# Kernel optimization log

Measured on AMD Instinct MI355X. Metric: run time of the kernel, lower is better.

## Reference

```python
import jax, jax.numpy as jnp
import numpy as np

NOPE = 128          # qk_nope_head_dim
ROPE = 64           # qk_rope_head_dim
KV_LORA = 512       # kv_lora_rank
SCALE = (KV_LORA + ROPE) ** (-0.5)


def setup_inputs() -> dict:
    key = jax.random.key(0)
    k1, k2, k3, k4, k5 = jax.random.split(key, 5)
    T, H, K, S = 512, 128, 512, 8192
    q = jax.random.normal(k1, (T, H, NOPE + ROPE), dtype=jnp.float32)
    kv_cache = jax.random.normal(k2, (S, KV_LORA + ROPE), dtype=jnp.float32)
    topk_indices = jax.random.randint(k3, (T, K), 0, S, dtype=jnp.int32)
    k_b_proj_trans = jax.random.normal(k4, (H, KV_LORA, NOPE), dtype=jnp.float32) * 0.02
    v_b_proj = jax.random.normal(k5, (H, 128, KV_LORA), dtype=jnp.float32) * 0.02
    return {"q": q, "kv_cache": kv_cache, "topk_indices": topk_indices,
            "k_b_proj_trans": k_b_proj_trans, "v_b_proj": v_b_proj}


def reference(q, kv_cache, topk_indices, k_b_proj_trans, v_b_proj):
    # q: [T, H, 192]; kv_cache: [S, 576]; topk_indices: [T, K]
    q_nope, q_rope = q[..., :NOPE], q[..., NOPE:]
    # bmm_out(q_nope_t, k_b_proj_trans.transpose(1,2)): [T,H,128] x [H,512,128] -> [T,H,512]
    q_lat = jnp.einsum('thd,hkd->thk', q_nope, k_b_proj_trans)
    q_concat = jnp.concatenate([q_lat, q_rope], axis=-1)        # [T, H, 576]
    # sparse MLA: gather selected latent KV per token
    kv_sel = kv_cache[topk_indices]                              # [T, K, 576]
    scores = jnp.einsum('thc,tkc->thk', q_concat, kv_sel) * SCALE
    p = jax.nn.softmax(scores, axis=-1)                          # [T, H, K]
    attn_lat = jnp.einsum('thk,tkc->thc', p, kv_sel[..., :KV_LORA])  # [T, H, 512]
    # bmm_out(attn_lat_t, v_b_proj.transpose(1,2)): [T,H,512] x [H,512,128] -> [T,H,128]
    out = jnp.einsum('thc,hvc->thv', attn_lat, v_b_proj)
    return out
```

## Files before the change

kernel.cpp:

```cpp
#include <hip/hip_runtime.h>
#include <stdint.h>


#define SCALE 0.041666666666666664f

typedef __bf16 bf16x8 __attribute__((ext_vector_type(8)));
typedef float floatx4 __attribute__((ext_vector_type(4)));
typedef unsigned int uint32x2 __attribute__((ext_vector_type(2)));
typedef unsigned int uint32x4 __attribute__((ext_vector_type(4)));

static __device__ __forceinline__ unsigned short f2bf(float f) {
  unsigned int u = __builtin_bit_cast(unsigned int, f);
  u += 0x7FFF + ((u >> 16) & 1);
  return (unsigned short)(u >> 16);
}
static __device__ __forceinline__ float bf2f(unsigned short h) {
  unsigned int u = ((unsigned int)h) << 16;
  return __builtin_bit_cast(float, u);
}
static __device__ __forceinline__ unsigned int pack2(float lo, float hi) {
  return (unsigned int)f2bf(lo) | ((unsigned int)f2bf(hi) << 16);
}
static __device__ __forceinline__ void ldsdma16(const void* g, void* l) {
  __builtin_amdgcn_global_load_lds(
      (const __attribute__((address_space(1))) void*)g,
      (__attribute__((address_space(3))) void*)l, 16, 0, 0);
}
static __device__ __forceinline__ unsigned int lds_addr(const void* p) {
  return (unsigned int)(unsigned long long)(
      (__attribute__((address_space(3))) const void*)p);
}
#define TR64(dst, addr, OFF) \
  asm volatile("ds_read_b64_tr_b16 %0, %1 offset:" OFF : "=v"(dst) : "v"(addr))

static __device__ __forceinline__ void stage8_f32(const float* __restrict__ src,
                                                  unsigned short* dst) {
  const float4* s4 = reinterpret_cast<const float4*>(src);
  float4 v0 = s4[0], v1 = s4[1];
  uint4 o;
  o.x = pack2(v0.x, v0.y); o.y = pack2(v0.z, v0.w);
  o.z = pack2(v1.x, v1.y); o.w = pack2(v1.z, v1.w);
  *reinterpret_cast<uint4*>(dst) = o;
}

static __device__ __forceinline__ void mfma_4x4(const unsigned short* As,
                                                const unsigned short* Bs,
                                                int wm, int wn, int l15, int quad,
                                                floatx4 acc[4][4]) {
  bf16x8 af[4], bfr[4];
#pragma unroll
  for (int i = 0; i < 4; ++i)
    af[i] = *reinterpret_cast<const bf16x8*>(&As[(wm + i * 16 + l15) * 32 + quad * 8]);
#pragma unroll
  for (int j = 0; j < 4; ++j)
    bfr[j] = *reinterpret_cast<const bf16x8*>(&Bs[(wn + j * 16 + l15) * 32 + quad * 8]);
#pragma unroll
  for (int i = 0; i < 4; ++i)
#pragma unroll
    for (int j = 0; j < 4; ++j)
      acc[i][j] = __builtin_amdgcn_mfma_f32_16x16x32_bf16(af[i], bfr[j], acc[i][j], 0, 0, 0);
}

__global__ void prep(const float* __restrict__ kv, unsigned short* __restrict__ kvb,
                     const float* __restrict__ q, unsigned short* __restrict__ qc) {
  int b = blockIdx.x;
  if (b < 4608) {
    int i = b * 256 + threadIdx.x;
    float4 v = reinterpret_cast<const float4*>(kv)[i];
    ushort4 o;
    o.x = f2bf(v.x); o.y = f2bf(v.y); o.z = f2bf(v.z); o.w = f2bf(v.w);
    reinterpret_cast<ushort4*>(kvb)[i] = o;
  } else {
    int i = (b - 4608) * 256 + threadIdx.x;
    int r = i & 63;
    int th = i >> 6;
    qc[(size_t)th * 576 + 512 + r] = f2bf(q[(size_t)th * 192 + 128 + r] * SCALE);
  }
}

__global__ __launch_bounds__(256) void qlat_gemm(const float* __restrict__ q,
                                                 const float* __restrict__ kb,
                                                 unsigned short* __restrict__ qc) {
  const int h = blockIdx.y;
  const int tm = (blockIdx.x & 3) * 128;
  const int tn = (blockIdx.x >> 2) * 128;
  __shared__ __align__(16) unsigned short As[128 * 32];
  __shared__ __align__(16) unsigned short Bs[128 * 32];
  const int tid = threadIdx.x;
  const int lane = tid & 63, wave = tid >> 6;
  const int wm = (wave & 1) * 64, wn = (wave >> 1) * 64;
  const int l15 = lane & 15, quad = lane >> 4;
  const int r0 = tid >> 2, cg = tid & 3;
  const float* a0 = q + ((size_t)(tm + r0) * 128 + h) * 192 + cg * 8;
  const float* a1 = q + ((size_t)(tm + r0 + 64) * 128 + h) * 192 + cg * 8;
  const float* b0 = kb + ((size_t)h * 512 + tn + r0) * 128 + cg * 8;
  const float* b1 = b0 + (size_t)64 * 128;
  floatx4 acc[4][4] = {};
  for (int ks = 0; ks < 4; ++ks) {
    stage8_f32(a0 + ks * 32, &As[tid * 8]);
    stage8_f32(a1 + ks * 32, &As[2048 + tid * 8]);
    stage8_f32(b0 + ks * 32, &Bs[tid * 8]);
    stage8_f32(b1 + ks * 32, &Bs[2048 + tid * 8]);
    __syncthreads();
    mfma_4x4(As, Bs, wm, wn, l15, quad, acc);
    __syncthreads();
  }
#pragma unroll
  for (int i = 0; i < 4; ++i) {
    const int row = wm + i * 16 + quad * 4;
#pragma unroll
    for (int j = 0; j < 4; ++j) {
      const int col = wn + j * 16 + l15;
#pragma unroll
      for (int r = 0; r < 4; ++r) {
        const int t = tm + row + r;
        qc[((size_t)t * 128 + h) * 576 + tn + col] = f2bf(acc[i][j][r] * SCALE);
      }
    }
  }
}

__global__ __launch_bounds__(256) void scores_gemm(const unsigned short* __restrict__ qc,
                                                   const unsigned short* __restrict__ kvb,
                                                   const int* __restrict__ topk,
                                                   unsigned short* __restrict__ P) {
  const int t = blockIdx.y;
  const int tn = blockIdx.x * 128;
  __shared__ __align__(16) unsigned short As[3][128 * 32];
  __shared__ __align__(16) unsigned short Bs[3][128 * 32];
  const int tid = threadIdx.x;
  const int lane = tid & 63, wave = tid >> 6;
  const int wm = (wave & 1) * 64, wn = (wave >> 1) * 64;
  const int l15 = lane & 15, quad = lane >> 4;
  const int r0 = tid >> 2, cg = tid & 3;
  const unsigned short* a0 = qc + ((size_t)t * 128 + r0) * 576 + cg * 8;
  const unsigned short* a1 = a0 + (size_t)64 * 576;
  const int idx0 = topk[t * 512 + tn + r0];
  const int idx1 = topk[t * 512 + tn + r0 + 64];
  const unsigned short* b0 = kvb + (size_t)idx0 * 576 + cg * 8;
  const unsigned short* b1 = kvb + (size_t)idx1 * 576 + cg * 8;
  floatx4 acc[4][4] = {};
#pragma unroll
  for (int p = 0; p < 2; ++p) {
    ldsdma16(a0 + p * 32, &As[p][tid * 8]);
    ldsdma16(a1 + p * 32, &As[p][2048 + tid * 8]);
    ldsdma16(b0 + p * 32, &Bs[p][tid * 8]);
    ldsdma16(b1 + p * 32, &Bs[p][2048 + tid * 8]);
  }
  int bi = 0, bn = 2;
  for (int ks = 0; ks < 18; ++ks) {
    if (ks < 16) {
      ldsdma16(a0 + (ks + 2) * 32, &As[bn][tid * 8]);
      ldsdma16(a1 + (ks + 2) * 32, &As[bn][2048 + tid * 8]);
      ldsdma16(b0 + (ks + 2) * 32, &Bs[bn][tid * 8]);
      ldsdma16(b1 + (ks + 2) * 32, &Bs[bn][2048 + tid * 8]);
      asm volatile("s_waitcnt vmcnt(8)" ::: "memory");
    } else if (ks == 16) {
      asm volatile("s_waitcnt vmcnt(4)" ::: "memory");
    } else {
      asm volatile("s_waitcnt vmcnt(0)" ::: "memory");
    }
    __builtin_amdgcn_s_barrier();
    mfma_4x4(As[bi], Bs[bi], wm, wn, l15, quad, acc);
    __builtin_amdgcn_s_barrier();
    bi = bi == 2 ? 0 : bi + 1;
    bn = bn == 2 ? 0 : bn + 1;
  }
#pragma unroll
  for (int i = 0; i < 4; ++i) {
    const int row = wm + i * 16 + quad * 4;
#pragma unroll
    for (int j = 0; j < 4; ++j) {
      const int col = tn + wn + j * 16 + l15;
#pragma unroll
      for (int r = 0; r < 4; ++r)
        P[((size_t)t * 128 + row + r) * 512 + col] = f2bf(acc[i][j][r]);
    }
  }
}

__global__ __launch_bounds__(256) void softmax_rows(const unsigned short* __restrict__ Pin,
                                                    unsigned short* __restrict__ P2) {
  const int row = blockIdx.x * 4 + (threadIdx.x >> 6);
  const int t = row >> 7, h = row & 127;
  const int lane = threadIdx.x & 63;
  const unsigned short* rp = Pin + (size_t)row * 512 + lane * 8;
  uint4 raw = *reinterpret_cast<const uint4*>(rp);
  unsigned int w[4] = {raw.x, raw.y, raw.z, raw.w};
  float f[8];
  float mx = -1e30f;
#pragma unroll
  for (int i = 0; i < 8; ++i) {
    f[i] = bf2f((unsigned short)((w[i >> 1] >> ((i & 1) * 16)) & 0xFFFF));
    mx = fmaxf(mx, f[i]);
  }
#pragma unroll
  for (int off = 32; off; off >>= 1) mx = fmaxf(mx, __shfl_xor(mx, off, 64));
  float s = 0.f;
#pragma unroll
  for (int i = 0; i < 8; ++i) { f[i] = __expf(f[i] - mx); s += f[i]; }
#pragma unroll
  for (int off = 32; off; off >>= 1) s += __shfl_xor(s, off, 64);
  const float inv = 1.0f / s;
  uint4 o;
  o.x = pack2(f[0] * inv, f[1] * inv);
  o.y = pack2(f[2] * inv, f[3] * inv);
  o.z = pack2(f[4] * inv, f[5] * inv);
  o.w = pack2(f[6] * inv, f[7] * inv);
  unsigned short* wp =
      P2 + (((size_t)t * 16 + (lane >> 2)) * 128 + h) * 32 + (lane & 3) * 8;
  *reinterpret_cast<uint4*>(wp) = o;
}

__global__ __launch_bounds__(512) void attn_gemm(const unsigned short* __restrict__ P2,
                                                 const unsigned short* __restrict__ kvb,
                                                 const int* __restrict__ topk,
                                                 unsigned short* __restrict__ alat) {
  const int t = blockIdx.x;
  __shared__ __align__(16) unsigned short St[3][32 * 512];
  const int tid = threadIdx.x;
  const int lane = tid & 63, wave = tid >> 6;
  const int wm = (wave >> 2) * 64;
  const int wc = wave & 3;
  const int l15 = lane & 15, quad = lane >> 4;
  const int keyBase = (tid >> 8) * 4 + ((tid >> 1) & 3);
  const int cA = ((tid >> 3) & 31) * 16 + (tid & 1) * 8;
  const int* tkrow = topk + t * 512;
  const unsigned short* a_base =
      P2 + ((size_t)t * 16 * 128 + wm + l15) * 32 + quad * 8;
  const unsigned int tra0 = lds_addr(&St[0][0]) + quad * 8192 + wc * 1024 + l15 * 8;
  floatx4 acc[4][8] = {};
  bf16x8 a_cur[4], a_nxt[4];
  int ip0, ip1, ip2, ip3;
  {
#pragma unroll
    for (int d = 0; d < 4; ++d) {
      const int k0 = tkrow[d * 8 + keyBase];
      ldsdma16(kvb + (size_t)k0 * 576 + cA, &St[0][d * 4096 + tid * 8]);
    }
#pragma unroll
    for (int i = 0; i < 4; ++i)
      a_cur[i] = *reinterpret_cast<const bf16x8*>(a_base + (size_t)i * 16 * 32);
    ip0 = tkrow[64 + 0 * 8 + keyBase];
    ip1 = tkrow[64 + 1 * 8 + keyBase];
    ip2 = tkrow[64 + 2 * 8 + keyBase];
    ip3 = tkrow[64 + 3 * 8 + keyBase];
#pragma unroll
    for (int d = 0; d < 4; ++d) {
      const int k1 = tkrow[32 + d * 8 + keyBase];
      ldsdma16(kvb + (size_t)k1 * 576 + cA, &St[1][d * 4096 + tid * 8]);
    }
  }
  int sti = 0, stp = 2;
  for (int ks = 0; ks < 16; ++ks) {
    asm volatile("s_waitcnt vmcnt(4)" ::: "memory");
    __builtin_amdgcn_s_barrier();
    const unsigned int tra = tra0 + sti * 32768;
    uint32x2 rl0, rl1, rl2, rl3, rl4, rl5, rl6, rl7;
    uint32x2 rh0, rh1, rh2, rh3, rh4, rh5, rh6, rh7;
    TR64(rl0, tra, "0");    TR64(rh0, tra, "4096");
    TR64(rl1, tra, "128");  TR64(rh1, tra, "4224");
    TR64(rl2, tra, "256");  TR64(rh2, tra, "4352");
    TR64(rl3, tra, "384");  TR64(rh3, tra, "4480");
    TR64(rl4, tra, "512");  TR64(rh4, tra, "4608");
    TR64(rl5, tra, "640");  TR64(rh5, tra, "4736");
    TR64(rl6, tra, "768");  TR64(rh6, tra, "4864");
    TR64(rl7, tra, "896");  TR64(rh7, tra, "4992");
    if (ks < 15) {
#pragma unroll
      for (int i = 0; i < 4; ++i)
        a_nxt[i] = *reinterpret_cast<const bf16x8*>(
            a_base + ((size_t)(ks + 1) * 128 + i * 16) * 32);
    }
    if (ks < 14) {
      const int d0 = ip0, d1 = ip1, d2 = ip2, d3 = ip3;
      if (ks < 13) {
        ip0 = tkrow[(ks + 3) * 32 + 0 * 8 + keyBase];
        ip1 = tkrow[(ks + 3) * 32 + 1 * 8 + keyBase];
        ip2 = tkrow[(ks + 3) * 32 + 2 * 8 + keyBase];
        ip3 = tkrow[(ks + 3) * 32 + 3 * 8 + keyBase];
      }
      ldsdma16(kvb + (size_t)d0 * 576 + cA, &St[stp][0 * 4096 + tid * 8]);
      ldsdma16(kvb + (size_t)d1 * 576 + cA, &St[stp][1 * 4096 + tid * 8]);
      ldsdma16(kvb + (size_t)d2 * 576 + cA, &St[stp][2 * 4096 + tid * 8]);
      ldsdma16(kvb + (size_t)d3 * 576 + cA, &St[stp][3 * 4096 + tid * 8]);
    }
    asm volatile("s_waitcnt lgkmcnt(0)");
    __builtin_amdgcn_sched_barrier(0);
    bf16x8 bfr[8];
    {
      uint32x4 w;
      w.x = rl0.x; w.y = rl0.y; w.z = rh0.x; w.w = rh0.y; bfr[0] = __builtin_bit_cast(bf16x8, w);
      w.x = rl1.x; w.y = rl1.y; w.z = rh1.x; w.w = rh1.y; bfr[1] = __builtin_bit_cast(bf16x8, w);
      w.x = rl2.x; w.y = rl2.y; w.z = rh2.x; w.w = rh2.y; bfr[2] = __builtin_bit_cast(bf16x8, w);
      w.x = rl3.x; w.y = rl3.y; w.z = rh3.x; w.w = rh3.y; bfr[3] = __builtin_bit_cast(bf16x8, w);
      w.x = rl4.x; w.y = rl4.y; w.z = rh4.x; w.w = rh4.y; bfr[4] = __builtin_bit_cast(bf16x8, w);
      w.x = rl5.x; w.y = rl5.y; w.z = rh5.x; w.w = rh5.y; bfr[5] = __builtin_bit_cast(bf16x8, w);
      w.x = rl6.x; w.y = rl6.y; w.z = rh6.x; w.w = rh6.y; bfr[6] = __builtin_bit_cast(bf16x8, w);
      w.x = rl7.x; w.y = rl7.y; w.z = rh7.x; w.w = rh7.y; bfr[7] = __builtin_bit_cast(bf16x8, w);
    }
#pragma unroll
    for (int i = 0; i < 4; ++i)
#pragma unroll
      for (int j = 0; j < 8; ++j)
        acc[i][j] =
            __builtin_amdgcn_mfma_f32_16x16x32_bf16(a_cur[i], bfr[j], acc[i][j], 0, 0, 0);
#pragma unroll
    for (int i = 0; i < 4; ++i) a_cur[i] = a_nxt[i];
    sti = sti == 2 ? 0 : sti + 1;
    stp = stp == 2 ? 0 : stp + 1;
  }
#pragma unroll
  for (int i = 0; i < 4; ++i) {
    const int row = wm + i * 16 + quad * 4;
#pragma unroll
    for (int j = 0; j < 8; ++j) {
      const int col = wc * 128 + j * 16 + l15;
#pragma unroll
      for (int r = 0; r < 4; ++r)
        alat[((size_t)(row + r) * 512 + t) * 512 + col] = f2bf(acc[i][j][r]);
    }
  }
}

__global__ __launch_bounds__(256) void out_gemm(const unsigned short* __restrict__ alat,
                                                const float* __restrict__ vb,
                                                float* __restrict__ out) {
  const int h = blockIdx.y;
  const int tm = blockIdx.x * 128;
  __shared__ __align__(16) unsigned short As[128 * 32];
  __shared__ __align__(16) unsigned short Bs[128 * 32];
  const int tid = threadIdx.x;
  const int lane = tid & 63, wave = tid >> 6;
  const int wm = (wave & 1) * 64, wn = (wave >> 1) * 64;
  const int l15 = lane & 15, quad = lane >> 4;
  const int r0 = tid >> 2, cg = tid & 3;
  const unsigned short* a0 = alat + ((size_t)h * 512 + tm + r0) * 512 + cg * 8;
  const unsigned short* a1 = a0 + (size_t)64 * 512;
  const float* b0 = vb + ((size_t)h * 128 + r0) * 512 + cg * 8;
  const float* b1 = b0 + (size_t)64 * 512;
  floatx4 acc[4][4] = {};
  for (int ks = 0; ks < 16; ++ks) {
    ldsdma16(a0 + ks * 32, &As[tid * 8]);
    ldsdma16(a1 + ks * 32, &As[2048 + tid * 8]);
    stage8_f32(b0 + ks * 32, &Bs[tid * 8]);
    stage8_f32(b1 + ks * 32, &Bs[2048 + tid * 8]);
    __syncthreads();
    mfma_4x4(As, Bs, wm, wn, l15, quad, acc);
    __syncthreads();
  }
#pragma unroll
  for (int i = 0; i < 4; ++i) {
    const int row = wm + i * 16 + quad * 4;
#pragma unroll
    for (int j = 0; j < 4; ++j) {
      const int col = wn + j * 16 + l15;
#pragma unroll
      for (int r = 0; r < 4; ++r) {
        const int t = tm + row + r;
        out[((size_t)t * 128 + h) * 128 + col] = acc[i][j][r];
      }
    }
  }
}

extern "C" void kernel_launch(void* const* d_in, const int* in_sizes, int n_in,
                              void* d_out, int out_size, void* d_ws, size_t ws_size,
                              hipStream_t stream) {
  const float* q = (const float*)d_in[0];
  const float* kv = (const float*)d_in[1];
  const int* topk = (const int*)d_in[2];
  const float* kb = (const float*)d_in[3];
  const float* vb = (const float*)d_in[4];
  float* out = (float*)d_out;

  char* ws = (char*)d_ws;
  unsigned short* kvb = (unsigned short*)ws;
  unsigned short* qc = (unsigned short*)(ws + 9437184);
  unsigned short* P = (unsigned short*)(ws + 9437184 + 75497472);
  unsigned short* P2 = qc;
  unsigned short* alat = P;

  prep<<<dim3(20992), dim3(256), 0, stream>>>(kv, kvb, q, qc);
  qlat_gemm<<<dim3(16, 128), dim3(256), 0, stream>>>(q, kb, qc);
  scores_gemm<<<dim3(4, 512), dim3(256), 0, stream>>>(qc, kvb, topk, P);
  softmax_rows<<<dim3(16384), dim3(256), 0, stream>>>(P, P2);
  attn_gemm<<<dim3(512), dim3(512), 0, stream>>>(P2, kvb, topk, alat);
  out_gemm<<<dim3(4, 128), dim3(256), 0, stream>>>(alat, vb, out);
}
```

Before: 383.9 us.

## Load A operands directly to registers in score/out GEMMs and swap grid order

In scores_gemm and out_gemm, the A operand is now read straight from global memory into registers in MFMA fragment layout instead of going through LDS, with scores_gemm prefetching the next k-slice one step ahead. This frees LDS and removes barrier traffic for A. Grid dimensions are transposed in qlat/scores/out so that consecutive blocks walk heads or tokens rather than tiles, which changes L2 locality. Scheduling fences are added around the DMA issue in attn_gemm. Direct global A loads are less coalesced and may raise VGPR pressure.

After: 402.2 us. +4.8%, slower.

```diff
diff --git a/kernel.cpp b/kernel.cpp
--- a/kernel.cpp
+++ b/kernel.cpp
@@ -25,6 +25,10 @@
   __builtin_amdgcn_global_load_lds(
       (const __attribute__((address_space(1))) void*)g,
       (__attribute__((address_space(3))) void*)l, 16, 0, 0);
+}
+static __device__ __forceinline__ void issue_fence() {
+  asm volatile("" ::: "memory");
+  __builtin_amdgcn_sched_barrier(0);
 }
 static __device__ __forceinline__ unsigned int lds_addr(const void* p) {
   return (unsigned int)(unsigned long long)(
@@ -81,9 +85,9 @@
 __global__ __launch_bounds__(256) void qlat_gemm(const float* __restrict__ q,
                                                  const float* __restrict__ kb,
                                                  unsigned short* __restrict__ qc) {
-  const int h = blockIdx.y;
-  const int tm = (blockIdx.x & 3) * 128;
-  const int tn = (blockIdx.x >> 2) * 128;
+  const int h = blockIdx.x;
+  const int tm = (blockIdx.y & 3) * 128;
+  const int tn = (blockIdx.y >> 2) * 128;
   __shared__ __align__(16) unsigned short As[128 * 32];
   __shared__ __align__(16) unsigned short Bs[128 * 32];
   const int tid = threadIdx.x;
@@ -124,45 +128,58 @@
                                                    const unsigned short* __restrict__ kvb,
                                                    const int* __restrict__ topk,
                                                    unsigned short* __restrict__ P) {
-  const int t = blockIdx.y;
-  const int tn = blockIdx.x * 128;
-  __shared__ __align__(16) unsigned short As[3][128 * 32];
+  const int t = blockIdx.x;
+  const int tn = blockIdx.y * 128;
   __shared__ __align__(16) unsigned short Bs[3][128 * 32];
   const int tid = threadIdx.x;
   const int lane = tid & 63, wave = tid >> 6;
   const int wm = (wave & 1) * 64, wn = (wave >> 1) * 64;
   const int l15 = lane & 15, quad = lane >> 4;
   const int r0 = tid >> 2, cg = tid & 3;
-  const unsigned short* a0 = qc + ((size_t)t * 128 + r0) * 576 + cg * 8;
-  const unsigned short* a1 = a0 + (size_t)64 * 576;
   const int idx0 = topk[t * 512 + tn + r0];
   const int idx1 = topk[t * 512 + tn + r0 + 64];
   const unsigned short* b0 = kvb + (size_t)idx0 * 576 + cg * 8;
   const unsigned short* b1 = kvb + (size_t)idx1 * 576 + cg * 8;
+  const unsigned short* aab = qc + ((size_t)t * 128 + wm + l15) * 576 + quad * 8;
   floatx4 acc[4][4] = {};
-#pragma unroll
-  for (int p = 0; p < 2; ++p) {
-    ldsdma16(a0 + p * 32, &As[p][tid * 8]);
-    ldsdma16(a1 + p * 32, &As[p][2048 + tid * 8]);
-    ldsdma16(b0 + p * 32, &Bs[p][tid * 8]);
-    ldsdma16(b1 + p * 32, &Bs[p][2048 + tid * 8]);
-  }
+  ldsdma16(b0, &Bs[0][tid * 8]);
+  ldsdma16(b1, &Bs[0][2048 + tid * 8]);
+  ldsdma16(b0 + 32, &Bs[1][tid * 8]);
+  ldsdma16(b1 + 32, &Bs[1][2048 + tid * 8]);
+  issue_fence();
+  bf16x8 af[4], an[4];
+#pragma unroll
+  for (int i = 0; i < 4; ++i)
+    af[i] = *reinterpret_cast<const bf16x8*>(aab + (size_t)i * 16 * 576);
   int bi = 0, bn = 2;
   for (int ks = 0; ks < 18; ++ks) {
+    asm volatile("s_waitcnt vmcnt(6)" ::: "memory");
+    __builtin_amdgcn_s_barrier();
     if (ks < 16) {
-      ldsdma16(a0 + (ks + 2) * 32, &As[bn][tid * 8]);
-      ldsdma16(a1 + (ks + 2) * 32, &As[bn][2048 + tid * 8]);
       ldsdma16(b0 + (ks + 2) * 32, &Bs[bn][tid * 8]);
       ldsdma16(b1 + (ks + 2) * 32, &Bs[bn][2048 + tid * 8]);
-      asm volatile("s_waitcnt vmcnt(8)" ::: "memory");
-    } else if (ks == 16) {
-      asm volatile("s_waitcnt vmcnt(4)" ::: "memory");
-    } else {
-      asm volatile("s_waitcnt vmcnt(0)" ::: "memory");
-    }
+      issue_fence();
+    }
+    if (ks < 17) {
+#pragma unroll
+      for (int i = 0; i < 4; ++i)
+        an[i] = *reinterpret_cast<const bf16x8*>(
+            aab + (ks + 1) * 32 + (size_t)i * 16 * 576);
+    }
+    bf16x8 bfr[4];
+#pragma unroll
+    for (int j = 0; j < 4; ++j)
+      bfr[j] = *reinterpret_cast<const bf16x8*>(
+          &Bs[bi][(wn + j * 16 + l15) * 32 + quad * 8]);
+#pragma unroll
+    for (int i = 0; i < 4; ++i)
+#pragma unroll
+      for (int j = 0; j < 4; ++j)
+        acc[i][j] =
+            __builtin_amdgcn_mfma_f32_16x16x32_bf16(af[i], bfr[j], acc[i][j], 0, 0, 0);
     __builtin_amdgcn_s_barrier();
-    mfma_4x4(As[bi], Bs[bi], wm, wn, l15, quad, acc);
-    __builtin_amdgcn_s_barrier();
+#pragma unroll
+    for (int i = 0; i < 4; ++i) af[i] = an[i];
     bi = bi == 2 ? 0 : bi + 1;
     bn = bn == 2 ? 0 : bn + 1;
   }
@@ -245,6 +262,7 @@
     ip1 = tkrow[64 + 1 * 8 + keyBase];
     ip2 = tkrow[64 + 2 * 8 + keyBase];
     ip3 = tkrow[64 + 3 * 8 + keyBase];
+    issue_fence();
 #pragma unroll
     for (int d = 0; d < 4; ++d) {
       const int k1 = tkrow[32 + d * 8 + keyBase];
@@ -280,6 +298,7 @@
         ip2 = tkrow[(ks + 3) * 32 + 2 * 8 + keyBase];
         ip3 = tkrow[(ks + 3) * 32 + 3 * 8 + keyBase];
       }
+      issue_fence();
       ldsdma16(kvb + (size_t)d0 * 576 + cA, &St[stp][0 * 4096 + tid * 8]);
       ldsdma16(kvb + (size_t)d1 * 576 + cA, &St[stp][1 * 4096 + tid * 8]);
       ldsdma16(kvb + (size_t)d2 * 576 + cA, &St[stp][2 * 4096 + tid * 8]);
@@ -326,27 +345,38 @@
 __global__ __launch_bounds__(256) void out_gemm(const unsigned short* __restrict__ alat,
                                                 const float* __restrict__ vb,
                                                 float* __restrict__ out) {
-  const int h = blockIdx.y;
-  const int tm = blockIdx.x * 128;
-  __shared__ __align__(16) unsigned short As[128 * 32];
+  const int h = blockIdx.x;
+  const int tm = blockIdx.y * 128;
   __shared__ __align__(16) unsigned short Bs[128 * 32];
   const int tid = threadIdx.x;
   const int lane = tid & 63, wave = tid >> 6;
   const int wm = (wave & 1) * 64, wn = (wave >> 1) * 64;
   const int l15 = lane & 15, quad = lane >> 4;
   const int r0 = tid >> 2, cg = tid & 3;
-  const unsigned short* a0 = alat + ((size_t)h * 512 + tm + r0) * 512 + cg * 8;
-  const unsigned short* a1 = a0 + (size_t)64 * 512;
+  const unsigned short* aab =
+      alat + ((size_t)h * 512 + tm + wm + l15) * 512 + quad * 8;
   const float* b0 = vb + ((size_t)h * 128 + r0) * 512 + cg * 8;
   const float* b1 = b0 + (size_t)64 * 512;
   floatx4 acc[4][4] = {};
   for (int ks = 0; ks < 16; ++ks) {
-    ldsdma16(a0 + ks * 32, &As[tid * 8]);
-    ldsdma16(a1 + ks * 32, &As[2048 + tid * 8]);
     stage8_f32(b0 + ks * 32, &Bs[tid * 8]);
     stage8_f32(b1 + ks * 32, &Bs[2048 + tid * 8]);
     __syncthreads();
-    mfma_4x4(As, Bs, wm, wn, l15, quad, acc);
+    bf16x8 af[4], bfr[4];
+#pragma unroll
+    for (int i = 0; i < 4; ++i)
+      af[i] = *reinterpret_cast<const bf16x8*>(
+          aab + ks * 32 + (size_t)i * 16 * 512);
+#pragma unroll
+    for (int j = 0; j < 4; ++j)
+      bfr[j] = *reinterpret_cast<const bf16x8*>(
+          &Bs[(wn + j * 16 + l15) * 32 + quad * 8]);
+#pragma unroll
+    for (int i = 0; i < 4; ++i)
+#pragma unroll
+      for (int j = 0; j < 4; ++j)
+        acc[i][j] =
+            __builtin_amdgcn_mfma_f32_16x16x32_bf16(af[i], bfr[j], acc[i][j], 0, 0, 0);
     __syncthreads();
   }
 #pragma unroll
@@ -382,9 +412,9 @@
   unsigned short* alat = P;
 
   prep<<<dim3(20992), dim3(256), 0, stream>>>(kv, kvb, q, qc);
-  qlat_gemm<<<dim3(16, 128), dim3(256), 0, stream>>>(q, kb, qc);
-  scores_gemm<<<dim3(4, 512), dim3(256), 0, stream>>>(qc, kvb, topk, P);
+  qlat_gemm<<<dim3(128, 16), dim3(256), 0, stream>>>(q, kb, qc);
+  scores_gemm<<<dim3(512, 4), dim3(256), 0, stream>>>(qc, kvb, topk, P);
   softmax_rows<<<dim3(16384), dim3(256), 0, stream>>>(P, P2);
   attn_gemm<<<dim3(512), dim3(512), 0, stream>>>(P2, kvb, topk, alat);
-  out_gemm<<<dim3(4, 128), dim3(256), 0, stream>>>(alat, vb, out);
-}
+  out_gemm<<<dim3(128, 4), dim3(256), 0, stream>>>(alat, vb, out);
+}
```
